# Performance work log

Measured on AMD Instinct MI355X. Metric: run time of the kernel, lower is better.

## Reference

```python
import jax, jax.numpy as jnp
import numpy as np

B, D, N = 1024, 2048, 16384
TEMP, LAMBDA2, MU = 0.05, 0.5, 1.0
EPS = 1e-12


def l2norm(x):
    # F.normalize(x, dim=1): x / max(||x||, eps)
    n = jnp.sqrt(jnp.sum(x * x, axis=1, keepdims=True))
    return x / jnp.maximum(n, EPS)


def cdist(x, f):
    # Euclidean distance matrix [B, N]
    x2 = jnp.sum(x * x, axis=1, keepdims=True)          # [B,1]
    f2 = jnp.sum(f * f, axis=1)                          # [N]
    sq = x2 + f2[None, :] - 2.0 * (x @ f.T)
    return jnp.sqrt(jnp.maximum(sq, 0.0))


def cross_entropy(logits, targets):
    logp = jax.nn.log_softmax(logits, axis=1)
    return -jnp.mean(logp[jnp.arange(logits.shape[0]), targets])


def setup_inputs() -> dict:
    key = jax.random.key(0)
    ks = jax.random.split(key, 10)
    inp = {
        'inputs': jax.random.normal(ks[0], (B, D), jnp.float32),
        'inputs_up': jax.random.normal(ks[1], (B, D), jnp.float32),
        'inputs_down': jax.random.normal(ks[2], (B, D), jnp.float32),
        'inputs_teacher': jax.random.normal(ks[3], (B, D), jnp.float32),
        'inputs_up_teacher': jax.random.normal(ks[4], (B, D), jnp.float32),
        'inputs_down_teacher': jax.random.normal(ks[5], (B, D), jnp.float32),
        'targets': jax.random.randint(ks[6], (B,), 0, N, jnp.int32),
        'epoch': 1,
        # memory bank buffers (unit-normalized rows, as maintained by CM updates)
        'features': l2norm(jax.random.normal(ks[7], (N, D), jnp.float32)),
        'features_up': l2norm(jax.random.normal(ks[8], (N, D), jnp.float32)),
        'features_down': l2norm(jax.random.normal(ks[9], (N, D), jnp.float32)),
    }
    return inp


def reference(inputs, inputs_up, inputs_down, inputs_teacher, inputs_up_teacher,
              inputs_down_teacher, targets, epoch, features, features_up, features_down):
    x = l2norm(inputs)
    xu = l2norm(inputs_up)
    xd = l2norm(inputs_down)
    t = l2norm(inputs_teacher)
    tu = l2norm(inputs_up_teacher)
    td = l2norm(inputs_down_teacher)

    # softmax over Euclidean distances to memory (used as 'logits' for CE below)
    x_soft = jax.nn.softmax(cdist(x, features), axis=1)
    xu_soft = jax.nn.softmax(cdist(xu, features_up), axis=1)
    xd_soft = jax.nn.softmax(cdist(xd, features_down), axis=1)

    # CM forward: similarity logits against memory, scaled by temperature
    out = (x @ features.T) / TEMP
    out_u = (xu @ features_up.T) / TEMP
    out_d = (xd @ features_down.T) / TEMP

    # MSELoss(reduce=False)(a,b).mean(0).sum()
    ld = jnp.sum(jnp.mean((x - t) ** 2, axis=0))
    ld_u = jnp.sum(jnp.mean((xu - tu) ** 2, axis=0))
    ld_d = jnp.sum(jnp.mean((xd - td) ** 2, axis=0))

    loss = ((1.0 - LAMBDA2) * (cross_entropy(out, targets) + MU * ld + cross_entropy(x_soft, targets))
            + LAMBDA2 * (cross_entropy(out_u, targets) + MU * ld_u + cross_entropy(xu_soft, targets))
            + LAMBDA2 * (cross_entropy(out_d, targets) + MU * ld_d + cross_entropy(xd_soft, targets)))
    return loss
```

## Files before the change

kernel.cpp:

```cpp
#include <hip/hip_runtime.h>

constexpr int BB = 1024;
constexpr int DD = 2048;
constexpr int NN = 16384;
constexpr float TEMP   = 0.05f;
constexpr float LAMBDA2 = 0.5f;
constexpr float MU      = 1.0f;
constexpr float EPSN    = 1e-12f;

typedef __bf16  bf16x8  __attribute__((ext_vector_type(8)));
typedef unsigned short ushort8 __attribute__((ext_vector_type(8)));
typedef float   floatx4 __attribute__((ext_vector_type(4)));

__device__ inline unsigned short f32_to_bf16(float f) {
  unsigned int u = __builtin_bit_cast(unsigned int, f);
  u += 0x7fffu + ((u >> 16) & 1u);
  return (unsigned short)(u >> 16);
}

__device__ inline float block_sum256(float v, float* sbuf) {
#pragma unroll
  for (int o = 32; o > 0; o >>= 1) v += __shfl_down(v, o, 64);
  int lane = threadIdx.x & 63, w = threadIdx.x >> 6;
  __syncthreads();
  if (lane == 0) sbuf[w] = v;
  __syncthreads();
  return sbuf[0] + sbuf[1] + sbuf[2] + sbuf[3];
}

__device__ inline float block_max256(float v, float* sbuf) {
#pragma unroll
  for (int o = 32; o > 0; o >>= 1) v = fmaxf(v, __shfl_down(v, o, 64));
  int lane = threadIdx.x & 63, w = threadIdx.x >> 6;
  __syncthreads();
  if (lane == 0) sbuf[w] = v;
  __syncthreads();
  return fmaxf(fmaxf(sbuf[0], sbuf[1]), fmaxf(sbuf[2], sbuf[3]));
}

__global__ void __launch_bounds__(256) norm_mse_kernel(
    const float* __restrict__ X, const float* __restrict__ T,
    unsigned short* __restrict__ Xb, float* __restrict__ mse_part) {
  __shared__ float sbuf[4];
  const int b = blockIdx.x;
  const float4* xr = (const float4*)(X + (size_t)b * DD);
  const float4* tr = (const float4*)(T + (size_t)b * DD);
  float4 xv[2], tv[2];
  float sx = 0.f, st = 0.f;
#pragma unroll
  for (int i = 0; i < 2; ++i) {
    int idx = i * 256 + threadIdx.x;
    xv[i] = xr[idx];  tv[i] = tr[idx];
    sx += xv[i].x*xv[i].x + xv[i].y*xv[i].y + xv[i].z*xv[i].z + xv[i].w*xv[i].w;
    st += tv[i].x*tv[i].x + tv[i].y*tv[i].y + tv[i].z*tv[i].z + tv[i].w*tv[i].w;
  }
  sx = block_sum256(sx, sbuf);
  st = block_sum256(st, sbuf);
  const float rx = 1.f / fmaxf(sqrtf(sx), EPSN);
  const float rt = 1.f / fmaxf(sqrtf(st), EPSN);
  float ms = 0.f;
  ushort4* xb4 = (ushort4*)(Xb + (size_t)b * DD);
#pragma unroll
  for (int i = 0; i < 2; ++i) {
    int idx = i * 256 + threadIdx.x;
    float xn, tn, d;
    ushort4 o;
    xn = xv[i].x * rx; tn = tv[i].x * rt; d = xn - tn; ms += d * d; o.x = f32_to_bf16(xn);
    xn = xv[i].y * rx; tn = tv[i].y * rt; d = xn - tn; ms += d * d; o.y = f32_to_bf16(xn);
    xn = xv[i].z * rx; tn = tv[i].z * rt; d = xn - tn; ms += d * d; o.z = f32_to_bf16(xn);
    xn = xv[i].w * rx; tn = tv[i].w * rt; d = xn - tn; ms += d * d; o.w = f32_to_bf16(xn);
    xb4[idx] = o;
  }
  ms = block_sum256(ms, sbuf);
  if (threadIdx.x == 0) mse_part[b] = ms;
}

__global__ void __launch_bounds__(256) feat_convert_kernel(
    const float* __restrict__ F, unsigned short* __restrict__ Fb) {
  const int stride = gridDim.x * 256;
  const float4* fr = (const float4*)F;
  constexpr int TOT = NN * DD / 8;
  for (int i = blockIdx.x * 256 + threadIdx.x; i < TOT; i += stride) {
    float4 a = fr[i * 2], b = fr[i * 2 + 1];
    ushort8 o;
    o[0] = f32_to_bf16(a.x); o[1] = f32_to_bf16(a.y);
    o[2] = f32_to_bf16(a.z); o[3] = f32_to_bf16(a.w);
    o[4] = f32_to_bf16(b.x); o[5] = f32_to_bf16(b.y);
    o[6] = f32_to_bf16(b.z); o[7] = f32_to_bf16(b.w);
    *(ushort8*)(Fb + (size_t)i * 8) = o;
  }
}

constexpr int BM = 256, BN = 256, BK = 64;
constexpr int KT = DD / BK;

__device__ inline void async_copy16(const void* g, void* l) {
  __builtin_amdgcn_global_load_lds(
      (const __attribute__((address_space(1))) unsigned int*)g,
      (__attribute__((address_space(3))) unsigned int*)l, 16, 0, 0);
}

__device__ __forceinline__ void stage_half(const unsigned short* src,
                                           unsigned short* dstRegion, int tid8) {
  async_copy16(src, dstRegion + tid8);
  async_copy16(src + 64 * DD, dstRegion + 4096 + tid8);
}

__global__ void __launch_bounds__(512, 2) gemm_bt_kernel(
    const unsigned short* __restrict__ A,
    const unsigned short* __restrict__ Bm,
    float* __restrict__ C) {
  __shared__ __align__(16) unsigned short As[2 * 2 * 128 * 64];
  __shared__ __align__(16) unsigned short Bs[2 * 2 * 128 * 64];

  const int tid  = threadIdx.x;
  const int lane = tid & 63;
  const int wave = tid >> 6;
  const int l16  = lane & 15;
  const int quad = lane >> 4;
  const int rm   = wave >> 2;
  const int rn   = wave & 3;
  const int m0 = blockIdx.y * BM;
  const int n0 = blockIdx.x * BN;

  const int xr = l16 & 7;
  const int cs[2] = { (quad ^ xr) * 8, ((4 + quad) ^ xr) * 8 };

  const int srow = tid >> 3;
  const int lcol = ((tid & 7) ^ (srow & 7)) * 8;
  const int tid8 = tid * 8;
  const unsigned short* aSrcT = A  + (size_t)(m0 + srow) * DD + lcol;
  const unsigned short* bSrcT = Bm + (size_t)(n0 + srow) * DD + lcol;

  floatx4 acc[8][4] = {};

  stage_half(aSrcT,                 As,         tid8);
  stage_half(aSrcT + 128 * DD,      As + 8192,  tid8);
  stage_half(bSrcT,                 Bs,         tid8);
  stage_half(bSrcT + 128 * DD,      Bs + 8192,  tid8);
  stage_half(bSrcT + BK,            Bs + 16384, tid8);
  stage_half(bSrcT + 128 * DD + BK, Bs + 24576, tid8);
  asm volatile("s_waitcnt vmcnt(4)" ::: "memory");
  asm volatile("s_barrier" ::: "memory");

  for (int i = 0; i < KT / 2; ++i) {
#pragma unroll
    for (int h = 0; h < 2; ++h) {
      const int t = 2 * i + h;
      unsigned short* Adst = As + (h ^ 1) * 16384;
      unsigned short* Bdst = Bs + h * 16384;
      const int kA = (t + 1 < KT) ? (t + 1) * BK : 0;
      const int kB = (t + 2 < KT) ? (t + 2) * BK : 0;
      const unsigned short* aS = aSrcT + kA;
      const unsigned short* bS = bSrcT + kB;
      const unsigned short* aB = As + h * 16384 + rm * 8192 + l16 * 64;
      const unsigned short* bB = Bs + h * 16384 + rn * 4096 + l16 * 64;

      bf16x8 bf[4][2];
#pragma unroll
      for (int mp = 0; mp < 4; ++mp) {
        if (mp == 0) {
#pragma unroll
          for (int n = 0; n < 4; ++n)
#pragma unroll
            for (int s = 0; s < 2; ++s)
              bf[n][s] = __builtin_bit_cast(bf16x8,
                           *(const ushort8*)(bB + n * 1024 + cs[s]));
        }
        bf16x8 af[2][2];
#pragma unroll
        for (int mi = 0; mi < 2; ++mi)
#pragma unroll
          for (int s = 0; s < 2; ++s)
            af[mi][s] = __builtin_bit_cast(bf16x8,
                          *(const ushort8*)(aB + (mp * 2 + mi) * 1024 + cs[s]));

        if      (mp == 0) stage_half(aS,            Adst,        tid8);
        else if (mp == 1) stage_half(aS + 128 * DD, Adst + 8192, tid8);
        else if (mp == 2) stage_half(bS,            Bdst,        tid8);
        else              stage_half(bS + 128 * DD, Bdst + 8192, tid8);

        asm volatile("s_barrier" ::: "memory");
        asm volatile("s_waitcnt lgkmcnt(0)" ::: "memory");
        __builtin_amdgcn_s_setprio(1);
#pragma unroll
        for (int mi = 0; mi < 2; ++mi)
#pragma unroll
          for (int n = 0; n < 4; ++n)
#pragma unroll
            for (int s = 0; s < 2; ++s)
              acc[mp * 2 + mi][n] = __builtin_amdgcn_mfma_f32_16x16x32_bf16(
                  af[mi][s], bf[n][s], acc[mp * 2 + mi][n], 0, 0, 0);
        __builtin_amdgcn_s_setprio(0);
        if (mp == 3)
          asm volatile("s_waitcnt vmcnt(4)" ::: "memory");
        asm volatile("s_barrier" ::: "memory");
      }
    }
  }

#pragma unroll
  for (int r = 0; r < 8; ++r) {
    const int grow = m0 + rm * 128 + r * 16 + quad * 4;
#pragma unroll
    for (int n = 0; n < 4; ++n) {
      const int gcol = n0 + rn * 64 + n * 16 + l16;
#pragma unroll
      for (int i = 0; i < 4; ++i)
        C[(size_t)(grow + i) * NN + gcol] = acc[r][n][i];
    }
  }
}

__global__ void __launch_bounds__(256) rowstat_kernel(
    const float* __restrict__ sim, const int* __restrict__ tgt,
    float* __restrict__ ce_part) {
  __shared__ float sbuf[4];
  const int b = blockIdx.x;
  const float4* sr = (const float4*)(sim + (size_t)b * NN);
  constexpr float INV_T = 1.0f / TEMP;

  float4 dv[16];
  float m1 = -1e30f, s1 = 0.f;
  float m2 = -1e30f;
#pragma unroll
  for (int i = 0; i < 16; ++i) {
    const int idx = i * 256 + threadIdx.x;
    float4 s = sr[idx];
    float lm = fmaxf(fmaxf(s.x, s.y), fmaxf(s.z, s.w)) * INV_T;
    if (lm > m1) { s1 *= expf(m1 - lm); m1 = lm; }
    s1 += expf(s.x * INV_T - m1) + expf(s.y * INV_T - m1)
        + expf(s.z * INV_T - m1) + expf(s.w * INV_T - m1);
    float4 d;
    d.x = sqrtf(fmaxf(2.f - 2.f * s.x, 0.f));
    d.y = sqrtf(fmaxf(2.f - 2.f * s.y, 0.f));
    d.z = sqrtf(fmaxf(2.f - 2.f * s.z, 0.f));
    d.w = sqrtf(fmaxf(2.f - 2.f * s.w, 0.f));
    dv[i] = d;
    m2 = fmaxf(m2, fmaxf(fmaxf(d.x, d.y), fmaxf(d.z, d.w)));
  }
  const float M1 = block_max256(m1, sbuf);
  const float s1t = block_sum256(s1 * expf(m1 - M1), sbuf);
  const float M2 = block_max256(m2, sbuf);

  float s2 = 0.f;
#pragma unroll
  for (int i = 0; i < 16; ++i) {
    float4 d = dv[i];
    s2 += expf(d.x - M2) + expf(d.y - M2) + expf(d.z - M2) + expf(d.w - M2);
  }
  const float s2t = block_sum256(s2, sbuf);
  const float invs2 = 1.f / s2t;

  float sp = 0.f;
#pragma unroll
  for (int i = 0; i < 16; ++i) {
    float4 d = dv[i];
    sp += expf(expf(d.x - M2) * invs2) + expf(expf(d.y - M2) * invs2)
        + expf(expf(d.z - M2) * invs2) + expf(expf(d.w - M2) * invs2);
  }
  const float spt = block_sum256(sp, sbuf);

  if (threadIdx.x == 0) {
    const int t = tgt[b];
    const float st = sim[(size_t)b * NN + t];
    const float dt = sqrtf(fmaxf(2.f - 2.f * st, 0.f));
    const float pt = expf(dt - M2) * invs2;
    const float ce1 = M1 + logf(s1t) - st * INV_T;
    const float ce2 = logf(spt) - pt;
    ce_part[b] = ce1 + ce2;
  }
}

__global__ void __launch_bounds__(256) final_reduce_kernel(
    const float* __restrict__ mse_part,
    const float* __restrict__ ce_part,
    float* __restrict__ loss) {
  __shared__ float sbuf[4];
  float s = 0.f;
  for (int i = threadIdx.x; i < 3 * BB; i += 256) {
    const float w = (i < BB) ? (1.0f - LAMBDA2) : LAMBDA2;
    s += w * (MU * mse_part[i] + ce_part[i]);
  }
  s = block_sum256(s, sbuf);
  if (threadIdx.x == 0) loss[0] = s * (1.0f / (float)BB);
}

extern "C" void kernel_launch(void* const* d_in, const int* in_sizes, int n_in,
                              void* d_out, int out_size, void* d_ws, size_t ws_size,
                              hipStream_t stream) {
  const float* xin[3] = {(const float*)d_in[0], (const float*)d_in[1], (const float*)d_in[2]};
  const float* tin[3] = {(const float*)d_in[3], (const float*)d_in[4], (const float*)d_in[5]};
  const int*   targets = (const int*)d_in[6];
  const float* fin[3] = {(const float*)d_in[8], (const float*)d_in[9], (const float*)d_in[10]};

  char* ws = (char*)d_ws;
  size_t off = 0;
  unsigned short* featb = (unsigned short*)(ws + off); off += (size_t)NN * DD * 2;
  float*          sim   = (float*)(ws + off);          off += (size_t)BB * NN * 4;
  unsigned short* xb    = (unsigned short*)(ws + off); off += (size_t)BB * DD * 2;
  float*          msep  = (float*)(ws + off);          off += (size_t)3 * BB * 4;
  float*          cep   = (float*)(ws + off);          off += (size_t)3 * BB * 4;

  for (int i = 0; i < 3; ++i) {
    norm_mse_kernel<<<BB, 256, 0, stream>>>(xin[i], tin[i], xb, msep + i * BB);
    feat_convert_kernel<<<4096, 256, 0, stream>>>(fin[i], featb);
    gemm_bt_kernel<<<dim3(NN / BN, BB / BM), 512, 0, stream>>>(xb, featb, sim);
    rowstat_kernel<<<BB, 256, 0, stream>>>(sim, targets, cep + i * BB);
  }
  final_reduce_kernel<<<1, 256, 0, stream>>>(msep, cep, (float*)d_out);
}
```

Before: 697.3 us.

## Batch the three branches into single launches per stage

Merges the three per-branch loops into one launch per stage (normalize, convert, GEMM with a z-dimension of 3, rowstat), using a larger workspace that holds all three branches' bf16 features, similarity matrices and normalized inputs. This is meant to cut launch count and fill the GPU better, especially the GEMM grid of 64x4 tiles, which is small for one branch. It needs about three times the workspace and falls back to the old sequential path when the workspace is too small. The extra working set may reduce cache reuse.

```diff
diff --git a/kernel.cpp b/kernel.cpp
--- a/kernel.cpp
+++ b/kernel.cpp
@@ -12,6 +12,10 @@
 typedef unsigned short ushort8 __attribute__((ext_vector_type(8)));
 typedef float   floatx4 __attribute__((ext_vector_type(4)));
 
+constexpr size_t F_SET   = (size_t)NN * DD;
+constexpr size_t X_SET   = (size_t)BB * DD;
+constexpr size_t SIM_SET = (size_t)BB * NN;
+
 __device__ inline unsigned short f32_to_bf16(float f) {
   unsigned int u = __builtin_bit_cast(unsigned int, f);
   u += 0x7fffu + ((u >> 16) & 1u);
@@ -38,11 +42,16 @@
   return fmaxf(fmaxf(sbuf[0], sbuf[1]), fmaxf(sbuf[2], sbuf[3]));
 }
 
-__global__ void __launch_bounds__(256) norm_mse_kernel(
-    const float* __restrict__ X, const float* __restrict__ T,
+__global__ void __launch_bounds__(256) norm_mse_all(
+    const float* __restrict__ X0, const float* __restrict__ X1, const float* __restrict__ X2,
+    const float* __restrict__ T0, const float* __restrict__ T1, const float* __restrict__ T2,
     unsigned short* __restrict__ Xb, float* __restrict__ mse_part) {
   __shared__ float sbuf[4];
-  const int b = blockIdx.x;
+  const int s = blockIdx.x >> 10;
+  const int b = blockIdx.x & (BB - 1);
+  const float* X = (s == 0) ? X0 : ((s == 1) ? X1 : X2);
+  const float* T = (s == 0) ? T0 : ((s == 1) ? T1 : T2);
+  unsigned short* xbp = Xb + (size_t)s * X_SET;
   const float4* xr = (const float4*)(X + (size_t)b * DD);
   const float4* tr = (const float4*)(T + (size_t)b * DD);
   float4 xv[2], tv[2];
@@ -59,7 +68,7 @@
   const float rx = 1.f / fmaxf(sqrtf(sx), EPSN);
   const float rt = 1.f / fmaxf(sqrtf(st), EPSN);
   float ms = 0.f;
-  ushort4* xb4 = (ushort4*)(Xb + (size_t)b * DD);
+  ushort4* xb4 = (ushort4*)(xbp + (size_t)b * DD);
 #pragma unroll
   for (int i = 0; i < 2; ++i) {
     int idx = i * 256 + threadIdx.x;
@@ -72,22 +81,27 @@
     xb4[idx] = o;
   }
   ms = block_sum256(ms, sbuf);
-  if (threadIdx.x == 0) mse_part[b] = ms;
-}
-
-__global__ void __launch_bounds__(256) feat_convert_kernel(
-    const float* __restrict__ F, unsigned short* __restrict__ Fb) {
-  const int stride = gridDim.x * 256;
+  if (threadIdx.x == 0) mse_part[s * BB + b] = ms;
+}
+
+__global__ void __launch_bounds__(256) feat_convert_all(
+    const float* __restrict__ F0, const float* __restrict__ F1, const float* __restrict__ F2,
+    unsigned short* __restrict__ Fb) {
+  const int s  = blockIdx.x >> 12;
+  const int lb = blockIdx.x & 4095;
+  const float* F = (s == 0) ? F0 : ((s == 1) ? F1 : F2);
+  unsigned short* fb = Fb + (size_t)s * F_SET;
   const float4* fr = (const float4*)F;
   constexpr int TOT = NN * DD / 8;
-  for (int i = blockIdx.x * 256 + threadIdx.x; i < TOT; i += stride) {
+  constexpr int STRIDE = 4096 * 256;
+  for (int i = lb * 256 + threadIdx.x; i < TOT; i += STRIDE) {
     float4 a = fr[i * 2], b = fr[i * 2 + 1];
     ushort8 o;
     o[0] = f32_to_bf16(a.x); o[1] = f32_to_bf16(a.y);
     o[2] = f32_to_bf16(a.z); o[3] = f32_to_bf16(a.w);
     o[4] = f32_to_bf16(b.x); o[5] = f32_to_bf16(b.y);
     o[6] = f32_to_bf16(b.z); o[7] = f32_to_bf16(b.w);
-    *(ushort8*)(Fb + (size_t)i * 8) = o;
+    *(ushort8*)(fb + (size_t)i * 8) = o;
   }
 }
 
@@ -106,12 +120,17 @@
   async_copy16(src + 64 * DD, dstRegion + 4096 + tid8);
 }
 
-__global__ void __launch_bounds__(512, 2) gemm_bt_kernel(
-    const unsigned short* __restrict__ A,
-    const unsigned short* __restrict__ Bm,
-    float* __restrict__ C) {
+__global__ void __launch_bounds__(512, 2) gemm_all(
+    const unsigned short* __restrict__ Ab,
+    const unsigned short* __restrict__ Fb,
+    float* __restrict__ Csim) {
   __shared__ __align__(16) unsigned short As[2 * 2 * 128 * 64];
   __shared__ __align__(16) unsigned short Bs[2 * 2 * 128 * 64];
+
+  const int set = blockIdx.z;
+  const unsigned short* A  = Ab + (size_t)set * X_SET;
+  const unsigned short* Bm = Fb + (size_t)set * F_SET;
+  float* C = Csim + (size_t)set * SIM_SET;
 
   const int tid  = threadIdx.x;
   const int lane = tid & 63;
@@ -212,12 +231,14 @@
   }
 }
 
-__global__ void __launch_bounds__(256) rowstat_kernel(
+__global__ void __launch_bounds__(256) rowstat_all(
     const float* __restrict__ sim, const int* __restrict__ tgt,
     float* __restrict__ ce_part) {
   __shared__ float sbuf[4];
-  const int b = blockIdx.x;
-  const float4* sr = (const float4*)(sim + (size_t)b * NN);
+  const int s = blockIdx.x >> 10;
+  const int b = blockIdx.x & (BB - 1);
+  const float* simp = sim + (size_t)s * SIM_SET;
+  const float4* sr = (const float4*)(simp + (size_t)b * NN);
   constexpr float INV_T = 1.0f / TEMP;
 
   float4 dv[16];
@@ -226,16 +247,16 @@
 #pragma unroll
   for (int i = 0; i < 16; ++i) {
     const int idx = i * 256 + threadIdx.x;
-    float4 s = sr[idx];
-    float lm = fmaxf(fmaxf(s.x, s.y), fmaxf(s.z, s.w)) * INV_T;
+    float4 sv = sr[idx];
+    float lm = fmaxf(fmaxf(sv.x, sv.y), fmaxf(sv.z, sv.w)) * INV_T;
     if (lm > m1) { s1 *= expf(m1 - lm); m1 = lm; }
-    s1 += expf(s.x * INV_T - m1) + expf(s.y * INV_T - m1)
-        + expf(s.z * INV_T - m1) + expf(s.w * INV_T - m1);
+    s1 += expf(sv.x * INV_T - m1) + expf(sv.y * INV_T - m1)
+        + expf(sv.z * INV_T - m1) + expf(sv.w * INV_T - m1);
     float4 d;
-    d.x = sqrtf(fmaxf(2.f - 2.f * s.x, 0.f));
-    d.y = sqrtf(fmaxf(2.f - 2.f * s.y, 0.f));
-    d.z = sqrtf(fmaxf(2.f - 2.f * s.z, 0.f));
-    d.w = sqrtf(fmaxf(2.f - 2.f * s.w, 0.f));
+    d.x = sqrtf(fmaxf(2.f - 2.f * sv.x, 0.f));
+    d.y = sqrtf(fmaxf(2.f - 2.f * sv.y, 0.f));
+    d.z = sqrtf(fmaxf(2.f - 2.f * sv.z, 0.f));
+    d.w = sqrtf(fmaxf(2.f - 2.f * sv.w, 0.f));
     dv[i] = d;
     m2 = fmaxf(m2, fmaxf(fmaxf(d.x, d.y), fmaxf(d.z, d.w)));
   }
@@ -263,12 +284,69 @@
 
   if (threadIdx.x == 0) {
     const int t = tgt[b];
-    const float st = sim[(size_t)b * NN + t];
+    const float st = simp[(size_t)b * NN + t];
     const float dt = sqrtf(fmaxf(2.f - 2.f * st, 0.f));
     const float pt = expf(dt - M2) * invs2;
     const float ce1 = M1 + logf(s1t) - st * INV_T;
     const float ce2 = logf(spt) - pt;
     ce_part[b] = ce1 + ce2;
+  }
+}
+
+__global__ void __launch_bounds__(256) rowstat_all_batched(
+    const float* __restrict__ sim, const int* __restrict__ tgt,
+    float* __restrict__ ce_part) {
+  __shared__ float sbuf[4];
+  const int s = blockIdx.x >> 10;
+  const int b = blockIdx.x & (BB - 1);
+  const float* simp = sim + (size_t)s * SIM_SET;
+  const float4* sr = (const float4*)(simp + (size_t)b * NN);
+  constexpr float INV_T = 1.0f / TEMP;
+  float4 dv[16];
+  float m1 = -1e30f, s1 = 0.f, m2 = -1e30f;
+#pragma unroll
+  for (int i = 0; i < 16; ++i) {
+    const int idx = i * 256 + threadIdx.x;
+    float4 sv = sr[idx];
+    float lm = fmaxf(fmaxf(sv.x, sv.y), fmaxf(sv.z, sv.w)) * INV_T;
+    if (lm > m1) { s1 *= expf(m1 - lm); m1 = lm; }
+    s1 += expf(sv.x * INV_T - m1) + expf(sv.y * INV_T - m1)
+        + expf(sv.z * INV_T - m1) + expf(sv.w * INV_T - m1);
+    float4 d;
+    d.x = sqrtf(fmaxf(2.f - 2.f * sv.x, 0.f));
+    d.y = sqrtf(fmaxf(2.f - 2.f * sv.y, 0.f));
+    d.z = sqrtf(fmaxf(2.f - 2.f * sv.z, 0.f));
+    d.w = sqrtf(fmaxf(2.f - 2.f * sv.w, 0.f));
+    dv[i] = d;
+    m2 = fmaxf(m2, fmaxf(fmaxf(d.x, d.y), fmaxf(d.z, d.w)));
+  }
+  const float M1 = block_max256(m1, sbuf);
+  const float s1t = block_sum256(s1 * expf(m1 - M1), sbuf);
+  const float M2 = block_max256(m2, sbuf);
+  float s2 = 0.f;
+#pragma unroll
+  for (int i = 0; i < 16; ++i) {
+    float4 d = dv[i];
+    s2 += expf(d.x - M2) + expf(d.y - M2) + expf(d.z - M2) + expf(d.w - M2);
+  }
+  const float s2t = block_sum256(s2, sbuf);
+  const float invs2 = 1.f / s2t;
+  float sp = 0.f;
+#pragma unroll
+  for (int i = 0; i < 16; ++i) {
+    float4 d = dv[i];
+    sp += expf(expf(d.x - M2) * invs2) + expf(expf(d.y - M2) * invs2)
+        + expf(expf(d.z - M2) * invs2) + expf(expf(d.w - M2) * invs2);
+  }
+  const float spt = block_sum256(sp, sbuf);
+  if (threadIdx.x == 0) {
+    const int t = tgt[b];
+    const float st = simp[(size_t)b * NN + t];
+    const float dt = sqrtf(fmaxf(2.f - 2.f * st, 0.f));
+    const float pt = expf(dt - M2) * invs2;
+    const float ce1 = M1 + logf(s1t) - st * INV_T;
+    const float ce2 = logf(spt) - pt;
+    ce_part[s * BB + b] = ce1 + ce2;
   }
 }
 
@@ -295,18 +373,38 @@
   const float* fin[3] = {(const float*)d_in[8], (const float*)d_in[9], (const float*)d_in[10]};
 
   char* ws = (char*)d_ws;
-  size_t off = 0;
-  unsigned short* featb = (unsigned short*)(ws + off); off += (size_t)NN * DD * 2;
-  float*          sim   = (float*)(ws + off);          off += (size_t)BB * NN * 4;
-  unsigned short* xb    = (unsigned short*)(ws + off); off += (size_t)BB * DD * 2;
-  float*          msep  = (float*)(ws + off);          off += (size_t)3 * BB * 4;
-  float*          cep   = (float*)(ws + off);          off += (size_t)3 * BB * 4;
-
-  for (int i = 0; i < 3; ++i) {
-    norm_mse_kernel<<<BB, 256, 0, stream>>>(xin[i], tin[i], xb, msep + i * BB);
-    feat_convert_kernel<<<4096, 256, 0, stream>>>(fin[i], featb);
-    gemm_bt_kernel<<<dim3(NN / BN, BB / BM), 512, 0, stream>>>(xb, featb, sim);
-    rowstat_kernel<<<BB, 256, 0, stream>>>(sim, targets, cep + i * BB);
-  }
-  final_reduce_kernel<<<1, 256, 0, stream>>>(msep, cep, (float*)d_out);
-}
+  const size_t needB = 3 * F_SET * 2 + 3 * SIM_SET * 4 + 3 * X_SET * 2
+                     + 2 * (size_t)3 * BB * 4;
+
+  if (ws_size >= needB) {
+    size_t off = 0;
+    unsigned short* featb = (unsigned short*)(ws + off); off += 3 * F_SET * 2;
+    float*          sim   = (float*)(ws + off);          off += 3 * SIM_SET * 4;
+    unsigned short* xb    = (unsigned short*)(ws + off); off += 3 * X_SET * 2;
+    float*          msep  = (float*)(ws + off);          off += (size_t)3 * BB * 4;
+    float*          cep   = (float*)(ws + off);          off += (size_t)3 * BB * 4;
+
+    norm_mse_all<<<3 * BB, 256, 0, stream>>>(
+        xin[0], xin[1], xin[2], tin[0], tin[1], tin[2], xb, msep);
+    feat_convert_all<<<3 * 4096, 256, 0, stream>>>(fin[0], fin[1], fin[2], featb);
+    gemm_all<<<dim3(NN / BN, BB / BM, 3), 512, 0, stream>>>(xb, featb, sim);
+    rowstat_all_batched<<<3 * BB, 256, 0, stream>>>(sim, targets, cep);
+    final_reduce_kernel<<<1, 256, 0, stream>>>(msep, cep, (float*)d_out);
+  } else {
+    size_t off = 0;
+    unsigned short* featb = (unsigned short*)(ws + off); off += F_SET * 2;
+    float*          sim   = (float*)(ws + off);          off += SIM_SET * 4;
+    unsigned short* xb    = (unsigned short*)(ws + off); off += X_SET * 2;
+    float*          msep  = (float*)(ws + off);          off += (size_t)3 * BB * 4;
+    float*          cep   = (float*)(ws + off);          off += (size_t)3 * BB * 4;
+
+    for (int i = 0; i < 3; ++i) {
+      norm_mse_all<<<BB, 256, 0, stream>>>(
+          xin[i], xin[i], xin[i], tin[i], tin[i], tin[i], xb, msep + i * BB);
+      feat_convert_all<<<4096, 256, 0, stream>>>(fin[i], fin[i], fin[i], featb);
+      gemm_all<<<dim3(NN / BN, BB / BM, 1), 512, 0, stream>>>(xb, featb, sim);
+      rowstat_all<<<BB, 256, 0, stream>>>(sim, targets, cep + i * BB);
+    }
+    final_reduce_kernel<<<1, 256, 0, stream>>>(msep, cep, (float*)d_out);
+  }
+}
```

Measured after the change: 733.4 us. 1.05x slower.
